# Performance work log

Measured on AMD Instinct MI355X. Metric: run time of the kernel, lower is better.

The kernel has to match this reference:

```python
import jax, jax.numpy as jnp
import numpy as np
import math

D_MODEL = 1024
EXPAND = 2
D_INNER = EXPAND * D_MODEL  # 2048
D_STATE = 16
D_CONV = 4
DT_RANK = math.ceil(D_MODEL / 16)  # 64
BATCH = 1
SEQLEN = 2048


def _silu(x):
    return x * jax.nn.sigmoid(x)


def _selective_scan(u, delta, A, B, C, D, z, delta_bias):
    """u, delta, z: (b,d,l); A: (d,n); B, C: (b,n,l); D, delta_bias: (d)."""
    delta = jax.nn.softplus(delta + delta_bias[None, :, None])        # (b,d,l)
    dA = jnp.exp(jnp.einsum('bdl,dn->lbdn', delta, A))                # (l,b,d,n)
    dBu = jnp.einsum('bdl,bnl->lbdn', delta * u, B)                   # (l,b,d,n)
    Ct = jnp.transpose(C, (2, 0, 1))                                  # (l,b,n)

    def step(h, inp):
        dA_t, dBu_t, C_t = inp
        h = dA_t * h + dBu_t                                          # (b,d,n)
        y = jnp.einsum('bdn,bn->bd', h, C_t)
        return h, y

    h0 = jnp.zeros((u.shape[0], u.shape[1], A.shape[1]), dtype=u.dtype)
    _, ys = jax.lax.scan(step, h0, (dA, dBu, Ct))                     # ys: (l,b,d)
    y = jnp.transpose(ys, (1, 2, 0))                                  # (b,d,l)
    y = y + D[:, None] * u
    return y * _silu(z)


def _causal_conv1d(x, conv_w, conv_b):
    """x: (b,d,l); conv_w: (d,w); conv_b: (d). Depthwise causal conv."""
    x_pad = jnp.pad(x, ((0, 0), (0, 0), (D_CONV - 1, 0)))
    kernel = conv_w[:, None, :]  # (d, 1, w)
    y = jax.lax.conv_general_dilated(
        x_pad, kernel, window_strides=(1,), padding='VALID',
        dimension_numbers=('NCH', 'OIH', 'NCH'),
        feature_group_count=D_INNER)
    return y + conv_b[None, :, None]


def setup_inputs() -> dict:
    key = jax.random.key(0)
    ks = jax.random.split(key, 12)
    hidden_states = jax.random.normal(ks[0], (BATCH, SEQLEN, D_MODEL), dtype=jnp.float32)
    in_proj_w = jax.random.normal(ks[1], (2 * D_INNER, D_MODEL), dtype=jnp.float32) * (D_MODEL ** -0.5)
    conv_w = jax.random.normal(ks[2], (D_INNER, D_CONV), dtype=jnp.float32) * (D_CONV ** -0.5)
    conv_b = jnp.zeros((D_INNER,), dtype=jnp.float32)
    dt_std = DT_RANK ** -0.5

    def dt_bias(k):
        dt = jnp.exp(jax.random.uniform(k, (D_INNER,)) * (math.log(0.1) - math.log(0.001)) + math.log(0.001))
        dt = jnp.clip(dt, 1e-4, None)
        return dt + jnp.log(-jnp.expm1(-dt))  # inverse softplus

    A_log = jnp.log(jnp.broadcast_to(jnp.arange(1, D_STATE + 1, dtype=jnp.float32), (D_INNER, D_STATE)))
    x1_proj_w = jax.random.normal(ks[3], (DT_RANK + 2 * D_STATE, D_INNER), dtype=jnp.float32) * (D_INNER ** -0.5)
    dt1_proj_w = jax.random.uniform(ks[4], (D_INNER, DT_RANK), minval=-dt_std, maxval=dt_std)
    dt1_proj_b = dt_bias(ks[5])
    x2_proj_w = jax.random.normal(ks[6], (DT_RANK + 2 * D_STATE, D_INNER), dtype=jnp.float32) * (D_INNER ** -0.5)
    dt2_proj_w = jax.random.uniform(ks[7], (D_INNER, DT_RANK), minval=-dt_std, maxval=dt_std)
    dt2_proj_b = dt_bias(ks[8])
    out_proj_w = jax.random.normal(ks[9], (D_MODEL, D_INNER), dtype=jnp.float32) * (D_INNER ** -0.5)
    return {
        'hidden_states': hidden_states,
        'in_proj_w': in_proj_w, 'conv_w': conv_w, 'conv_b': conv_b,
        'x1_proj_w': x1_proj_w, 'dt1_proj_w': dt1_proj_w, 'dt1_proj_b': dt1_proj_b,
        'A1_log': A_log, 'D1': jnp.ones((D_INNER,), dtype=jnp.float32),
        'x2_proj_w': x2_proj_w, 'dt2_proj_w': dt2_proj_w, 'dt2_proj_b': dt2_proj_b,
        'A2_log': A_log, 'D2': jnp.ones((D_INNER,), dtype=jnp.float32),
        'out_proj_w': out_proj_w,
    }


def reference(hidden_states, in_proj_w, conv_w, conv_b,
              x1_proj_w, dt1_proj_w, dt1_proj_b, A1_log, D1,
              x2_proj_w, dt2_proj_w, dt2_proj_b, A2_log, D2,
              out_proj_w):
    # in_proj: (b,l,d) @ W^T -> (b, 2*d_inner, l)
    xz = jnp.einsum('bld,ed->bel', hidden_states, in_proj_w)
    x, z = jnp.split(xz, 2, axis=1)                                   # (b,d_inner,l) each
    A1 = -jnp.exp(A1_log.astype(jnp.float32))
    A2 = -jnp.exp(A2_log.astype(jnp.float32))
    x = _silu(_causal_conv1d(x, conv_w, conv_b))                      # (b,d_inner,l)

    def branch_params(xp_w, dtp_w):
        dbl = jnp.einsum('bdl,kd->bkl', x, xp_w)                      # (b, r+2n, l)
        dt, Bm, Cm = jnp.split(dbl, [DT_RANK, DT_RANK + D_STATE], axis=1)
        dt = jnp.einsum('brl,dr->bdl', dt, dtp_w)
        return dt, Bm, Cm

    dt1, B1, C1 = branch_params(x1_proj_w, dt1_proj_w)
    dt2, B2, C2 = branch_params(x2_proj_w, dt2_proj_w)
    y1 = _selective_scan(x, dt1, A1, B1, C1, D1.astype(jnp.float32), z, dt1_proj_b.astype(jnp.float32))
    y2 = _selective_scan(x, dt2, A2, B2, C2, D2.astype(jnp.float32), z, dt2_proj_b.astype(jnp.float32))
    y = y1 - y2                                                       # (b,d_inner,l)
    out = jnp.einsum('bdl,od->blo', y, out_proj_w)                    # (b,l,d_model)
    return out
```

## Files before the change

kernel.cpp:

```cpp
#include <hip/hip_runtime.h>
#include <math.h>

#define SEQ 2048
#define DMODEL 1024
#define DIN 2048
#define NST 16
#define DTR 64
#define CH 64
#define NCH (SEQ / CH)

typedef __attribute__((ext_vector_type(8))) short bf16x8;
typedef __attribute__((ext_vector_type(4))) float f32x4;

__device__ __forceinline__ ushort f2bf(float f) {
  union { float f; unsigned u; } c; c.f = f;
  return (ushort)((c.u + 0x7fffu + ((c.u >> 16) & 1u)) >> 16);
}
__device__ __forceinline__ float bf2f(ushort h) {
  union { unsigned u; float f; } c; c.u = ((unsigned)h) << 16;
  return c.f;
}
__device__ __forceinline__ float splus(float v) {
  return v > 20.f ? v : log1pf(__expf(v));
}
__device__ __forceinline__ void powers16(float e, float* p) {
  float e2 = e * e, e4 = e2 * e2, e8 = e4 * e4;
  p[0] = e;       p[1] = e2;       p[2] = e2 * e;   p[3] = e4;
  p[4] = e4 * e;  p[5] = e4 * e2;  p[6] = e4 * p[2]; p[7] = e8;
  p[8] = e8 * e;  p[9] = e8 * e2;  p[10] = e8 * p[2]; p[11] = e8 * e4;
  p[12] = e8 * p[4]; p[13] = e8 * p[5]; p[14] = e8 * p[6]; p[15] = e8 * e8;
}

#define GLL(g, l) __builtin_amdgcn_global_load_lds( \
    (const __attribute__((address_space(1))) void*)(g), \
    (__attribute__((address_space(3))) void*)(l), 16, 0, 0)

template<int BM, int BN, int SPLITK>
__global__ __launch_bounds__(256) void gemm3p(const ushort* __restrict__ Ahi,
                                              const ushort* __restrict__ Alo,
                                              const ushort* __restrict__ Bhi,
                                              const ushort* __restrict__ Blo,
                                              float* __restrict__ C,
                                              int M, int N, int K) {
  constexpr int BK = 32;
  constexpr int WM = BM / 2, WN = BN / 2, TM = WM / 16, TN = WN / 16;
  constexpr int SA = BM / 16, SB = BN / 16;
  __shared__ __align__(16) ushort sAh[BM * BK], sAl[BM * BK];
  __shared__ __align__(16) ushort sBh[BN * BK], sBl[BN * BK];
  const int tid = threadIdx.x, wid = tid >> 6, lane = tid & 63;
  const int m0 = blockIdx.y * BM, n0 = blockIdx.x * BN;
  const int Kc = K / SPLITK, kbeg = blockIdx.z * Kc;
  const int wm0 = (wid >> 1) * WM, wn0 = (wid & 1) * WN;
  const int fr = lane & 15;
  const int lrow = lane >> 2;
  const int lkc = (lane & 3) ^ ((lane >> 3) & 3);
  const int fpo = fr * 32 + (((lane >> 4) ^ ((lane >> 1) & 3)) * 8);

  f32x4 acc[TM][TN];
#pragma unroll
  for (int mi = 0; mi < TM; ++mi)
#pragma unroll
    for (int ni = 0; ni < TN; ++ni)
#pragma unroll
      for (int r = 0; r < 4; ++r) acc[mi][ni][r] = 0.f;

  for (int k0 = 0; k0 < Kc; k0 += BK) {
    __syncthreads();
    const int kg = kbeg + k0 + lkc * 8;
#pragma unroll
    for (int i = 0; i < SA / 4; ++i) {
      const int seg = wid * (SA / 4) + i;
      const size_t ga = (size_t)(m0 + seg * 16 + lrow) * K + kg;
      GLL(&Ahi[ga], &sAh[seg * 512]);
      GLL(&Alo[ga], &sAl[seg * 512]);
    }
#pragma unroll
    for (int i = 0; i < SB / 4; ++i) {
      const int seg = wid * (SB / 4) + i;
      const size_t ga = (size_t)(n0 + seg * 16 + lrow) * K + kg;
      GLL(&Bhi[ga], &sBh[seg * 512]);
      GLL(&Blo[ga], &sBl[seg * 512]);
    }
    __syncthreads();

    bf16x8 ah[TM], al[TM], bh[TN], bl[TN];
#pragma unroll
    for (int mi = 0; mi < TM; ++mi) {
      const int r = (wm0 / 16 + mi) * 512 + fpo;
      ah[mi] = *(const bf16x8*)&sAh[r];
      al[mi] = *(const bf16x8*)&sAl[r];
    }
#pragma unroll
    for (int ni = 0; ni < TN; ++ni) {
      const int r = (wn0 / 16 + ni) * 512 + fpo;
      bh[ni] = *(const bf16x8*)&sBh[r];
      bl[ni] = *(const bf16x8*)&sBl[r];
    }
#pragma unroll
    for (int mi = 0; mi < TM; ++mi)
#pragma unroll
      for (int ni = 0; ni < TN; ++ni) {
        acc[mi][ni] = __builtin_amdgcn_mfma_f32_16x16x32_bf16(ah[mi], bh[ni], acc[mi][ni], 0, 0, 0);
        acc[mi][ni] = __builtin_amdgcn_mfma_f32_16x16x32_bf16(ah[mi], bl[ni], acc[mi][ni], 0, 0, 0);
        acc[mi][ni] = __builtin_amdgcn_mfma_f32_16x16x32_bf16(al[mi], bh[ni], acc[mi][ni], 0, 0, 0);
      }
  }

  float* __restrict__ Co = C + (size_t)blockIdx.z * M * N;
#pragma unroll
  for (int mi = 0; mi < TM; ++mi)
#pragma unroll
    for (int ni = 0; ni < TN; ++ni)
#pragma unroll
      for (int r = 0; r < 4; ++r)
        Co[(size_t)(m0 + wm0 + mi * 16 + (lane >> 4) * 4 + r) * N + n0 + wn0 + ni * 16 + fr] =
            acc[mi][ni][r];
}

__device__ __forceinline__ void split_store4(float4 v, ushort* hi, ushort* lo, size_t i) {
  ushort h0 = f2bf(v.x), h1 = f2bf(v.y), h2 = f2bf(v.z), h3 = f2bf(v.w);
  *(ushort4*)&hi[i] = make_ushort4(h0, h1, h2, h3);
  *(ushort4*)&lo[i] = make_ushort4(f2bf(v.x - bf2f(h0)), f2bf(v.y - bf2f(h1)),
                                   f2bf(v.z - bf2f(h2)), f2bf(v.w - bf2f(h3)));
}

__global__ __launch_bounds__(256) void cvt_fused(const float* __restrict__ inw,
                                                 const float* __restrict__ hid,
                                                 const float* __restrict__ x1w,
                                                 const float* __restrict__ x2w,
                                                 ushort* __restrict__ w_hi, ushort* __restrict__ w_lo,
                                                 ushort* __restrict__ h_hi, ushort* __restrict__ h_lo,
                                                 ushort* __restrict__ wx_hi, ushort* __restrict__ wx_lo) {
  const int q = blockIdx.x * 256 + threadIdx.x;
  const float* src; ushort* dhi; ushort* dlo; int base;
  if (q < 1048576)            { src = inw; dhi = w_hi;  dlo = w_lo;  base = q; }
  else if (q < 1572864)       { src = hid; dhi = h_hi;  dlo = h_lo;  base = q - 1048576; }
  else if (q < 1622016)       { src = x1w; dhi = wx_hi; dlo = wx_lo; base = q - 1572864; }
  else                        { src = x2w; dhi = wx_hi + 196608; dlo = wx_lo + 196608; base = q - 1622016; }
  const size_t i = (size_t)base * 4;
  split_store4(*(const float4*)&src[i], dhi, dlo, i);
}

__global__ __launch_bounds__(256) void cvt_split(const float* __restrict__ x,
                                                 ushort* __restrict__ hi,
                                                 ushort* __restrict__ lo, int n) {
  const int i = (blockIdx.x * 256 + threadIdx.x) * 4;
  if (i >= n) return;
  split_store4(*(const float4*)&x[i], hi, lo, i);
}

__global__ __launch_bounds__(256) void reduce_out(const float* __restrict__ p,
                                                  float* __restrict__ o, int n) {
  const int i = (blockIdx.x * 256 + threadIdx.x) * 4;
  if (i >= n) return;
  float4 a = *(const float4*)&p[i];
  float4 b = *(const float4*)&p[(size_t)n + i];
  float4 c = *(const float4*)&p[(size_t)2 * n + i];
  float4 d = *(const float4*)&p[(size_t)3 * n + i];
  *(float4*)&o[i] = make_float4(a.x + b.x + c.x + d.x, a.y + b.y + c.y + d.y,
                                a.z + b.z + c.z + d.z, a.w + b.w + c.w + d.w);
}

__global__ __launch_bounds__(256) void conv_tr_kernel(const float* __restrict__ xz,
                                                      const float* __restrict__ cw,
                                                      const float* __restrict__ cb,
                                                      ushort* __restrict__ xcT_hi,
                                                      ushort* __restrict__ xcT_lo) {
  const int l0 = blockIdx.x * 64, d0 = blockIdx.y * 64;
  const int tid = threadIdx.x;
  __shared__ float xin[64][68];
  __shared__ float To[64][65];
  __shared__ float cwS[64][4];
  __shared__ float cbS[64];

  for (int i = tid; i < 1024; i += 256) {
    const int d = i >> 4, q = i & 15;
    float4 v = *(const float4*)&xz[(size_t)(d0 + d) * SEQ + l0 + q * 4];
    xin[d][3 + q * 4 + 0] = v.x; xin[d][3 + q * 4 + 1] = v.y;
    xin[d][3 + q * 4 + 2] = v.z; xin[d][3 + q * 4 + 3] = v.w;
  }
  if (tid < 192) {
    const int j = tid >> 6, d = tid & 63;
    const int l = l0 - 3 + j;
    xin[d][j] = (l >= 0) ? xz[(size_t)(d0 + d) * SEQ + l] : 0.f;
  }
  if (tid < 64) {
    cbS[tid] = cb[d0 + tid];
    float4 w = *(const float4*)&cw[(d0 + tid) * 4];
    cwS[tid][0] = w.x; cwS[tid][1] = w.y; cwS[tid][2] = w.z; cwS[tid][3] = w.w;
  }
  __syncthreads();

  for (int i = tid; i < 4096; i += 256) {
    const int d = i >> 6, l = i & 63;
    float a = cbS[d] + cwS[d][0] * xin[d][l] + cwS[d][1] * xin[d][l + 1] +
              cwS[d][2] * xin[d][l + 2] + cwS[d][3] * xin[d][l + 3];
    To[d][l] = a / (1.f + __expf(-a));
  }
  __syncthreads();

  for (int i = tid; i < 4096; i += 256) {
    const int l = i >> 6, dd = i & 63;
    float v = To[dd][l];
    ushort h = f2bf(v);
    xcT_hi[(size_t)(l0 + l) * DIN + d0 + dd] = h;
    xcT_lo[(size_t)(l0 + l) * DIN + d0 + dd] = f2bf(v - bf2f(h));
  }
}

__global__ __launch_bounds__(256) void ydiff_tr_kernel(const float* __restrict__ y1,
                                                       const float* __restrict__ y2,
                                                       const float* __restrict__ xz,
                                                       ushort* __restrict__ hi,
                                                       ushort* __restrict__ lo) {
  const int l0 = blockIdx.x * 64, d0 = blockIdx.y * 64;
  const int tid = threadIdx.x;
  __shared__ float Tz[64][65];
  for (int i = tid; i < 1024; i += 256) {
    const int d = i >> 4, q = i & 15;
    float4 v = *(const float4*)&xz[(size_t)(DIN + d0 + d) * SEQ + l0 + q * 4];
    Tz[d][q * 4 + 0] = v.x / (1.f + __expf(-v.x));
    Tz[d][q * 4 + 1] = v.y / (1.f + __expf(-v.y));
    Tz[d][q * 4 + 2] = v.z / (1.f + __expf(-v.z));
    Tz[d][q * 4 + 3] = v.w / (1.f + __expf(-v.w));
  }
  __syncthreads();
  for (int i = tid; i < 1024; i += 256) {
    const int l = i >> 4, dc = (i & 15) * 4;
    const size_t g = (size_t)(l0 + l) * DIN + d0 + dc;
    float4 a = *(const float4*)&y1[g];
    float4 b = *(const float4*)&y2[g];
    float4 v = make_float4((a.x - b.x) * Tz[dc + 0][l], (a.y - b.y) * Tz[dc + 1][l],
                           (a.z - b.z) * Tz[dc + 2][l], (a.w - b.w) * Tz[dc + 3][l]);
    split_store4(v, hi, lo, g);
  }
}

__global__ __launch_bounds__(256) void reduce_dblS_kernel(const float* __restrict__ p,
                                                          float* __restrict__ o,
                                                          float* __restrict__ BT1,
                                                          float* __restrict__ CT1,
                                                          float* __restrict__ BT2,
                                                          float* __restrict__ CT2) {
  const int NE = 192 * SEQ;
  const int idx = blockIdx.x * 256 + threadIdx.x;
  float s = 0.f;
#pragma unroll
  for (int cc = 0; cc < 8; ++cc) s += p[(size_t)cc * NE + idx];
  o[idx] = s;
  const int k = idx >> 11, l = idx & (SEQ - 1);
  if (k >= 64 && k < 80)        BT1[l * NST + (k - 64)] = s;
  else if (k >= 80 && k < 96)   CT1[l * NST + (k - 80)] = s;
  else if (k >= 160 && k < 176) BT2[l * NST + (k - 160)] = s;
  else if (k >= 176)            CT2[l * NST + (k - 176)] = s;
}

__global__ __launch_bounds__(256) void dt_gemm_kernel(const float* __restrict__ dbl1,
                                                      const float* __restrict__ dbl2,
                                                      const float* __restrict__ w1,
                                                      const float* __restrict__ w2,
                                                      const float* __restrict__ b1,
                                                      const float* __restrict__ b2,
                                                      float* __restrict__ o1,
                                                      float* __restrict__ o2) {
  const int br = blockIdx.z;
  const float* __restrict__ dbl = br ? dbl2 : dbl1;
  const float* __restrict__ W = br ? w2 : w1;
  const float* __restrict__ dtb = br ? b2 : b1;
  float* __restrict__ outp = br ? o2 : o1;
  const int l0 = blockIdx.x * 64, d0 = blockIdx.y * 64;
  __shared__ __align__(16) float Wt[64][68];
  __shared__ __align__(16) float Bs[64][68];
  const int tid = threadIdx.x;
  for (int i = tid; i < 4096; i += 256) {
    int a = i >> 6, b = i & 63;
    Wt[b][a] = W[(size_t)(d0 + a) * DTR + b];
    Bs[a][b] = dbl[(size_t)a * SEQ + l0 + b];
  }
  __syncthreads();
  const int tl_ = tid >> 4, td_ = tid & 15;
  float acc[4][4];
#pragma unroll
  for (int i = 0; i < 4; ++i)
#pragma unroll
    for (int j = 0; j < 4; ++j) acc[i][j] = 0.f;
  for (int r = 0; r < 64; ++r) {
    float4 av = *(const float4*)&Bs[r][tl_ * 4];
    float4 bv = *(const float4*)&Wt[r][td_ * 4];
    float am[4] = {av.x, av.y, av.z, av.w};
    float bn[4] = {bv.x, bv.y, bv.z, bv.w};
#pragma unroll
    for (int i = 0; i < 4; ++i)
#pragma unroll
      for (int j = 0; j < 4; ++j) acc[i][j] = fmaf(am[i], bn[j], acc[i][j]);
  }
  const float4 bias4 = *(const float4*)&dtb[d0 + td_ * 4];
#pragma unroll
  for (int i = 0; i < 4; ++i) {
    float4 w = make_float4(splus(acc[i][0] + bias4.x), splus(acc[i][1] + bias4.y),
                           splus(acc[i][2] + bias4.z), splus(acc[i][3] + bias4.w));
    *(float4*)&outp[(size_t)(l0 + tl_ * 4 + i) * DIN + d0 + td_ * 4] = w;
  }
}

__global__ __launch_bounds__(256) void scan_phase_a(const ushort* __restrict__ uhi,
                                                    const ushort* __restrict__ ulo,
                                                    const float* __restrict__ sp1T,
                                                    const float* __restrict__ sp2T,
                                                    const float* __restrict__ BT1,
                                                    const float* __restrict__ BT2,
                                                    const float* __restrict__ Al1,
                                                    const float* __restrict__ Al2,
                                                    float* __restrict__ hend,
                                                    float* __restrict__ Pend) {
  const int br = blockIdx.z;
  const float* __restrict__ spp = br ? sp2T : sp1T;
  const float* __restrict__ BT = br ? BT2 : BT1;
  const float* __restrict__ Al = br ? Al2 : Al1;
  const int c = blockIdx.y;
  const int t0 = c * CH;
  const int d = blockIdx.x * 256 + threadIdx.x;
  const size_t gbase = (size_t)t0 * DIN + d;

  __shared__ __align__(16) float Bs[CH][NST];
  ((float4*)Bs)[threadIdx.x] = ((const float4*)&BT[t0 * NST])[threadIdx.x];
  __syncthreads();

  bool fast = true;
#pragma unroll
  for (int n = 0; n < NST; ++n) {
    float kx = __expf(Al[(size_t)d * NST + n]);
    fast = fast && (fabsf(kx - (float)(n + 1)) < 1e-3f);
  }
  float h[NST];
#pragma unroll
  for (int n = 0; n < NST; ++n) h[n] = 0.f;
  float S = 0.f;

  if (fast) {
    for (int tt = 0; tt < CH / 4; ++tt) {
      float sparr[4], uarr[4];
#pragma unroll
      for (int j = 0; j < 4; ++j) {
        const size_t idx = gbase + (size_t)(tt * 4 + j) * DIN;
        sparr[j] = spp[idx];
        uarr[j] = bf2f(uhi[idx]) + bf2f(ulo[idx]);
      }
#pragma unroll
      for (int j = 0; j < 4; ++j) {
        const int t = tt * 4 + j;
        const float sp = sparr[j];
        S += sp;
        const float spu = sp * uarr[j];
        const float e = __expf(-sp);
        float p[NST];
        powers16(e, p);
#pragma unroll
        for (int ng = 0; ng < 4; ++ng) {
          float4 bq = *(const float4*)&Bs[t][ng * 4];
          float bf[4] = {bq.x, bq.y, bq.z, bq.w};
#pragma unroll
          for (int k = 0; k < 4; ++k) {
            int n = ng * 4 + k;
            h[n] = fmaf(p[n], h[n], spu * bf[k]);
          }
        }
      }
    }
  } else {
    float AnL2[NST];
#pragma unroll
    for (int n = 0; n < NST; ++n)
      AnL2[n] = -__expf(Al[(size_t)d * NST + n]) * 1.4426950408889634f;
    for (int tt = 0; tt < CH / 4; ++tt) {
      float sparr[4], uarr[4];
#pragma unroll
      for (int j = 0; j < 4; ++j) {
        const size_t idx = gbase + (size_t)(tt * 4 + j) * DIN;
        sparr[j] = spp[idx];
        uarr[j] = bf2f(uhi[idx]) + bf2f(ulo[idx]);
      }
#pragma unroll
      for (int j = 0; j < 4; ++j) {
        const int t = tt * 4 + j;
        const float sp = sparr[j];
        S += sp;
        const float spu = sp * uarr[j];
#pragma unroll
        for (int ng = 0; ng < 4; ++ng) {
          float4 bq = *(const float4*)&Bs[t][ng * 4];
          float bf[4] = {bq.x, bq.y, bq.z, bq.w};
#pragma unroll
          for (int k = 0; k < 4; ++k) {
            int n = ng * 4 + k;
            float dA = exp2f(AnL2[n] * sp);
            h[n] = fmaf(dA, h[n], spu * bf[k]);
          }
        }
      }
    }
  }

  float P[NST];
  if (fast) {
    powers16(__expf(-S), P);
  } else {
#pragma unroll
    for (int n = 0; n < NST; ++n)
      P[n] = exp2f(-__expf(Al[(size_t)d * NST + n]) * 1.4426950408889634f * S);
  }
  size_t base = ((size_t)(br * NCH + c) * DIN + d) * NST;
#pragma unroll
  for (int n = 0; n < NST; n += 4) {
    *(float4*)&hend[base + n] = make_float4(h[n], h[n + 1], h[n + 2], h[n + 3]);
    *(float4*)&Pend[base + n] = make_float4(P[n], P[n + 1], P[n + 2], P[n + 3]);
  }
}

__global__ __launch_bounds__(256) void scan_carry(const float* __restrict__ hend,
                                                  float* __restrict__ PendHin) {
  const int flat = blockIdx.x * 256 + threadIdx.x;
  const int br = flat >> 15;
  const int dn = flat & 32767;
  float h = 0.f;
  for (int c = 0; c < NCH; ++c) {
    size_t idx = ((size_t)(br * NCH + c) << 15) + dn;
    float Pv = PendHin[idx];
    float he = hend[idx];
    PendHin[idx] = h;
    h = fmaf(Pv, h, he);
  }
}

__global__ __launch_bounds__(256) void scan_phase_c(const ushort* __restrict__ uhi,
                                                    const ushort* __restrict__ ulo,
                                                    const float* __restrict__ sp1T,
                                                    const float* __restrict__ sp2T,
                                                    const float* __restrict__ BT1,
                                                    const float* __restrict__ CT1,
                                                    const float* __restrict__ BT2,
                                                    const float* __restrict__ CT2,
                                                    const float* __restrict__ Al1,
                                                    const float* __restrict__ Al2,
                                                    const float* __restrict__ D1,
                                                    const float* __restrict__ D2,
                                                    const float* __restrict__ hin,
                                                    float* __restrict__ y1t,
                                                    float* __restrict__ y2t) {
  const int br = blockIdx.z;
  const float* __restrict__ spp = br ? sp2T : sp1T;
  const float* __restrict__ BT = br ? BT2 : BT1;
  const float* __restrict__ CT = br ? CT2 : CT1;
  const float* __restrict__ Al = br ? Al2 : Al1;
  const float* __restrict__ Dp = br ? D2 : D1;
  float* __restrict__ yt = br ? y2t : y1t;
  const int c = blockIdx.y;
  const int t0 = c * CH;
  const int d = blockIdx.x * 256 + threadIdx.x;
  const size_t gbase = (size_t)t0 * DIN + d;

  __shared__ __align__(16) float Bs[CH][NST];
  __shared__ __align__(16) float Cs[CH][NST];
  ((float4*)Bs)[threadIdx.x] = ((const float4*)&BT[t0 * NST])[threadIdx.x];
  ((float4*)Cs)[threadIdx.x] = ((const float4*)&CT[t0 * NST])[threadIdx.x];
  __syncthreads();

  bool fast = true;
#pragma unroll
  for (int n = 0; n < NST; ++n) {
    float kx = __expf(Al[(size_t)d * NST + n]);
    fast = fast && (fabsf(kx - (float)(n + 1)) < 1e-3f);
  }
  const float Dd = Dp[d];
  float h[NST];
  const size_t hbase = ((size_t)(br * NCH + c) * DIN + d) * NST;
#pragma unroll
  for (int n = 0; n < NST; n += 4) {
    float4 hv = *(const float4*)&hin[hbase + n];
    h[n] = hv.x; h[n + 1] = hv.y; h[n + 2] = hv.z; h[n + 3] = hv.w;
  }

  if (fast) {
    for (int tt = 0; tt < CH / 4; ++tt) {
      float sparr[4], uarr[4];
#pragma unroll
      for (int j = 0; j < 4; ++j) {
        const size_t idx = gbase + (size_t)(tt * 4 + j) * DIN;
        sparr[j] = spp[idx];
        uarr[j] = bf2f(uhi[idx]) + bf2f(ulo[idx]);
      }
#pragma unroll
      for (int j = 0; j < 4; ++j) {
        const int t = tt * 4 + j;
        const float sp = sparr[j];
        const float spu = sp * uarr[j];
        const float e = __expf(-sp);
        float p[NST];
        powers16(e, p);
        float y = 0.f;
#pragma unroll
        for (int ng = 0; ng < 4; ++ng) {
          float4 bq = *(const float4*)&Bs[t][ng * 4];
          float4 cq = *(const float4*)&Cs[t][ng * 4];
          float bf[4] = {bq.x, bq.y, bq.z, bq.w};
          float cf[4] = {cq.x, cq.y, cq.z, cq.w};
#pragma unroll
          for (int k = 0; k < 4; ++k) {
            int n = ng * 4 + k;
            h[n] = fmaf(p[n], h[n], spu * bf[k]);
            y = fmaf(h[n], cf[k], y);
          }
        }
        yt[gbase + (size_t)t * DIN] = y + Dd * uarr[j];
      }
    }
  } else {
    float AnL2[NST];
#pragma unroll
    for (int n = 0; n < NST; ++n)
      AnL2[n] = -__expf(Al[(size_t)d * NST + n]) * 1.4426950408889634f;
    for (int tt = 0; tt < CH / 4; ++tt) {
      float sparr[4], uarr[4];
#pragma unroll
      for (int j = 0; j < 4; ++j) {
        const size_t idx = gbase + (size_t)(tt * 4 + j) * DIN;
        sparr[j] = spp[idx];
        uarr[j] = bf2f(uhi[idx]) + bf2f(ulo[idx]);
      }
#pragma unroll
      for (int j = 0; j < 4; ++j) {
        const int t = tt * 4 + j;
        const float sp = sparr[j];
        const float spu = sp * uarr[j];
        float y = 0.f;
#pragma unroll
        for (int ng = 0; ng < 4; ++ng) {
          float4 bq = *(const float4*)&Bs[t][ng * 4];
          float4 cq = *(const float4*)&Cs[t][ng * 4];
          float bf[4] = {bq.x, bq.y, bq.z, bq.w};
          float cf[4] = {cq.x, cq.y, cq.z, cq.w};
#pragma unroll
          for (int k = 0; k < 4; ++k) {
            int n = ng * 4 + k;
            float dA = exp2f(AnL2[n] * sp);
            h[n] = fmaf(dA, h[n], spu * bf[k]);
            y = fmaf(h[n], cf[k], y);
          }
        }
        yt[gbase + (size_t)t * DIN] = y + Dd * uarr[j];
      }
    }
  }
}

extern "C" void kernel_launch(void* const* d_in, const int* in_sizes, int n_in,
                              void* d_out, int out_size, void* d_ws, size_t ws_size,
                              hipStream_t stream) {
  const float* hidden = (const float*)d_in[0];
  const float* in_proj_w = (const float*)d_in[1];
  const float* conv_w = (const float*)d_in[2];
  const float* conv_b = (const float*)d_in[3];
  const float* x1w = (const float*)d_in[4];
  const float* dtw1 = (const float*)d_in[5];
  const float* dtb1 = (const float*)d_in[6];
  const float* Al1 = (const float*)d_in[7];
  const float* D1 = (const float*)d_in[8];
  const float* x2w = (const float*)d_in[9];
  const float* dtw2 = (const float*)d_in[10];
  const float* dtb2 = (const float*)d_in[11];
  const float* Al2 = (const float*)d_in[12];
  const float* D2 = (const float*)d_in[13];
  const float* outw = (const float*)d_in[14];
  float* out = (float*)d_out;

  float* ws = (float*)d_ws;
  float* xz = ws;
  float* xcTbuf = xz + (size_t)4096 * SEQ;
  float* dblS = xcTbuf + (size_t)SEQ * DIN;
  float* sp1T = dblS + (size_t)192 * SEQ;
  float* sp2T = sp1T + (size_t)SEQ * DIN;
  float* y1t = sp2T + (size_t)SEQ * DIN;
  float* y2t = y1t + (size_t)SEQ * DIN;
  float* hend = y2t + (size_t)SEQ * DIN;
  float* Pend = hend + (size_t)2 * NCH * DIN * NST;
  float* BT1 = Pend + (size_t)2 * NCH * DIN * NST;
  float* CT1 = BT1 + (size_t)SEQ * NST;
  float* BT2 = CT1 + (size_t)SEQ * NST;
  float* CT2 = BT2 + (size_t)SEQ * NST;
  float* wxp = CT2 + (size_t)SEQ * NST;

  float* dbl1 = dblS;
  float* dbl2 = dblS + (size_t)96 * SEQ;

  ushort* xcT_hi = (ushort*)xcTbuf;
  ushort* xcT_lo = (ushort*)(xcTbuf + 2097152);
  ushort* w_hi = (ushort*)y1t;
  ushort* w_lo = (ushort*)(y1t + 2097152);
  ushort* h_hi = (ushort*)y2t;
  ushort* h_lo = (ushort*)(y2t + 1048576);
  ushort* wx_hi = (ushort*)wxp;
  ushort* wx_lo = (ushort*)(wxp + 196608);
  float* xp_part = sp1T;
  ushort* yd_hi = (ushort*)xcTbuf;
  ushort* yd_lo = (ushort*)(xcTbuf + 2097152);
  ushort* ow_hi = (ushort*)hend;
  ushort* ow_lo = (ushort*)(hend + 1048576);
  float* opart = xz;

  dim3 blk(256);

  cvt_fused<<<dim3(6528), blk, 0, stream>>>(in_proj_w, hidden, x1w, x2w,
                                            w_hi, w_lo, h_hi, h_lo, wx_hi, wx_lo);

  gemm3p<128, 128, 1><<<dim3(SEQ / 128, 4096 / 128, 1), blk, 0, stream>>>(
      w_hi, w_lo, h_hi, h_lo, xz, 4096, SEQ, DMODEL);

  conv_tr_kernel<<<dim3(SEQ / 64, DIN / 64), blk, 0, stream>>>(
      xz, conv_w, conv_b, xcT_hi, xcT_lo);

  gemm3p<64, 128, 8><<<dim3(SEQ / 128, 192 / 64, 8), blk, 0, stream>>>(
      wx_hi, wx_lo, xcT_hi, xcT_lo, xp_part, 192, SEQ, DIN);

  reduce_dblS_kernel<<<dim3(192 * SEQ / 256), blk, 0, stream>>>(
      xp_part, dblS, BT1, CT1, BT2, CT2);

  dt_gemm_kernel<<<dim3(SEQ / 64, DIN / 64, 2), blk, 0, stream>>>(
      dbl1, dbl2, dtw1, dtw2, dtb1, dtb2, sp1T, sp2T);

  scan_phase_a<<<dim3(DIN / 256, NCH, 2), blk, 0, stream>>>(
      xcT_hi, xcT_lo, sp1T, sp2T, BT1, BT2, Al1, Al2, hend, Pend);
  scan_carry<<<dim3(2 * DIN * NST / 256), blk, 0, stream>>>(hend, Pend);
  cvt_split<<<dim3(2048), blk, 0, stream>>>(outw, ow_hi, ow_lo, DMODEL * DIN);
  scan_phase_c<<<dim3(DIN / 256, NCH, 2), blk, 0, stream>>>(
      xcT_hi, xcT_lo, sp1T, sp2T, BT1, CT1, BT2, CT2, Al1, Al2, D1, D2, Pend, y1t, y2t);

  ydiff_tr_kernel<<<dim3(SEQ / 64, DIN / 64), blk, 0, stream>>>(
      y1t, y2t, xz, yd_hi, yd_lo);

  gemm3p<128, 128, 4><<<dim3(DMODEL / 128, SEQ / 128, 4), blk, 0, stream>>>(
      yd_hi, yd_lo, ow_hi, ow_lo, opart, SEQ, DMODEL, DIN);
  reduce_out<<<dim3(SEQ * DMODEL / 1024), blk, 0, stream>>>(opart, out, SEQ * DMODEL);
}
```

Baseline: 334.8 us.

## Fuse both scan branches with y-difference and gating into one phase-c kernel

The two selective-scan branches are computed in the same thread in one kernel, which also applies the y1-y2 difference, the silu(z) gate and the bf16 hi/lo split. This removes the y1/y2 intermediate round trip and the separate ydiff kernel. A new z transpose kernel precomputes silu(z) in (l,d) layout. The cost is half as many blocks and roughly doubled register pressure per thread.

```diff
diff --git a/kernel.cpp b/kernel.cpp
--- a/kernel.cpp
+++ b/kernel.cpp
@@ -208,11 +208,8 @@
   }
 }
 
-__global__ __launch_bounds__(256) void ydiff_tr_kernel(const float* __restrict__ y1,
-                                                       const float* __restrict__ y2,
-                                                       const float* __restrict__ xz,
-                                                       ushort* __restrict__ hi,
-                                                       ushort* __restrict__ lo) {
+__global__ __launch_bounds__(256) void z_tr_kernel(const float* __restrict__ xz,
+                                                   float* __restrict__ zT) {
   const int l0 = blockIdx.x * 64, d0 = blockIdx.y * 64;
   const int tid = threadIdx.x;
   __shared__ float Tz[64][65];
@@ -227,12 +224,8 @@
   __syncthreads();
   for (int i = tid; i < 1024; i += 256) {
     const int l = i >> 4, dc = (i & 15) * 4;
-    const size_t g = (size_t)(l0 + l) * DIN + d0 + dc;
-    float4 a = *(const float4*)&y1[g];
-    float4 b = *(const float4*)&y2[g];
-    float4 v = make_float4((a.x - b.x) * Tz[dc + 0][l], (a.y - b.y) * Tz[dc + 1][l],
-                           (a.z - b.z) * Tz[dc + 2][l], (a.w - b.w) * Tz[dc + 3][l]);
-    split_store4(v, hi, lo, g);
+    *(float4*)&zT[(size_t)(l0 + l) * DIN + d0 + dc] =
+        make_float4(Tz[dc + 0][l], Tz[dc + 1][l], Tz[dc + 2][l], Tz[dc + 3][l]);
   }
 }
 
@@ -432,122 +425,143 @@
   }
 }
 
-__global__ __launch_bounds__(256) void scan_phase_c(const ushort* __restrict__ uhi,
-                                                    const ushort* __restrict__ ulo,
-                                                    const float* __restrict__ sp1T,
-                                                    const float* __restrict__ sp2T,
-                                                    const float* __restrict__ BT1,
-                                                    const float* __restrict__ CT1,
-                                                    const float* __restrict__ BT2,
-                                                    const float* __restrict__ CT2,
-                                                    const float* __restrict__ Al1,
-                                                    const float* __restrict__ Al2,
-                                                    const float* __restrict__ D1,
-                                                    const float* __restrict__ D2,
-                                                    const float* __restrict__ hin,
-                                                    float* __restrict__ y1t,
-                                                    float* __restrict__ y2t) {
-  const int br = blockIdx.z;
-  const float* __restrict__ spp = br ? sp2T : sp1T;
-  const float* __restrict__ BT = br ? BT2 : BT1;
-  const float* __restrict__ CT = br ? CT2 : CT1;
-  const float* __restrict__ Al = br ? Al2 : Al1;
-  const float* __restrict__ Dp = br ? D2 : D1;
-  float* __restrict__ yt = br ? y2t : y1t;
+__global__ __launch_bounds__(256) void scan_phase_c_fused(
+    const ushort* __restrict__ uhi, const ushort* __restrict__ ulo,
+    const float* __restrict__ sp1T, const float* __restrict__ sp2T,
+    const float* __restrict__ BT1, const float* __restrict__ CT1,
+    const float* __restrict__ BT2, const float* __restrict__ CT2,
+    const float* __restrict__ Al1, const float* __restrict__ Al2,
+    const float* __restrict__ D1, const float* __restrict__ D2,
+    const float* __restrict__ hin, const float* __restrict__ zT,
+    ushort* __restrict__ yd_hi, ushort* __restrict__ yd_lo) {
   const int c = blockIdx.y;
   const int t0 = c * CH;
   const int d = blockIdx.x * 256 + threadIdx.x;
   const size_t gbase = (size_t)t0 * DIN + d;
 
-  __shared__ __align__(16) float Bs[CH][NST];
-  __shared__ __align__(16) float Cs[CH][NST];
-  ((float4*)Bs)[threadIdx.x] = ((const float4*)&BT[t0 * NST])[threadIdx.x];
-  ((float4*)Cs)[threadIdx.x] = ((const float4*)&CT[t0 * NST])[threadIdx.x];
+  __shared__ __align__(16) float Bs1[CH][NST], Cs1[CH][NST];
+  __shared__ __align__(16) float Bs2[CH][NST], Cs2[CH][NST];
+  ((float4*)Bs1)[threadIdx.x] = ((const float4*)&BT1[t0 * NST])[threadIdx.x];
+  ((float4*)Cs1)[threadIdx.x] = ((const float4*)&CT1[t0 * NST])[threadIdx.x];
+  ((float4*)Bs2)[threadIdx.x] = ((const float4*)&BT2[t0 * NST])[threadIdx.x];
+  ((float4*)Cs2)[threadIdx.x] = ((const float4*)&CT2[t0 * NST])[threadIdx.x];
   __syncthreads();
 
   bool fast = true;
 #pragma unroll
   for (int n = 0; n < NST; ++n) {
-    float kx = __expf(Al[(size_t)d * NST + n]);
-    fast = fast && (fabsf(kx - (float)(n + 1)) < 1e-3f);
-  }
-  const float Dd = Dp[d];
-  float h[NST];
-  const size_t hbase = ((size_t)(br * NCH + c) * DIN + d) * NST;
+    float k1 = __expf(Al1[(size_t)d * NST + n]);
+    float k2 = __expf(Al2[(size_t)d * NST + n]);
+    fast = fast && (fabsf(k1 - (float)(n + 1)) < 1e-3f) &&
+           (fabsf(k2 - (float)(n + 1)) < 1e-3f);
+  }
+  const float Dd1 = D1[d], Dd2 = D2[d];
+  float h1[NST], h2[NST];
+  const size_t hb1 = ((size_t)c * DIN + d) * NST;
+  const size_t hb2 = ((size_t)(NCH + c) * DIN + d) * NST;
 #pragma unroll
   for (int n = 0; n < NST; n += 4) {
-    float4 hv = *(const float4*)&hin[hbase + n];
-    h[n] = hv.x; h[n + 1] = hv.y; h[n + 2] = hv.z; h[n + 3] = hv.w;
+    float4 v1 = *(const float4*)&hin[hb1 + n];
+    float4 v2 = *(const float4*)&hin[hb2 + n];
+    h1[n] = v1.x; h1[n + 1] = v1.y; h1[n + 2] = v1.z; h1[n + 3] = v1.w;
+    h2[n] = v2.x; h2[n + 1] = v2.y; h2[n + 2] = v2.z; h2[n + 3] = v2.w;
   }
 
   if (fast) {
     for (int tt = 0; tt < CH / 4; ++tt) {
-      float sparr[4], uarr[4];
+      float sp1a[4], sp2a[4], uarr[4], zarr[4];
 #pragma unroll
       for (int j = 0; j < 4; ++j) {
         const size_t idx = gbase + (size_t)(tt * 4 + j) * DIN;
-        sparr[j] = spp[idx];
+        sp1a[j] = sp1T[idx];
+        sp2a[j] = sp2T[idx];
         uarr[j] = bf2f(uhi[idx]) + bf2f(ulo[idx]);
+        zarr[j] = zT[idx];
       }
 #pragma unroll
       for (int j = 0; j < 4; ++j) {
         const int t = tt * 4 + j;
-        const float sp = sparr[j];
-        const float spu = sp * uarr[j];
-        const float e = __expf(-sp);
-        float p[NST];
-        powers16(e, p);
-        float y = 0.f;
+        const float uu = uarr[j];
+        const float spu1 = sp1a[j] * uu, spu2 = sp2a[j] * uu;
+        float p1[NST], p2[NST];
+        powers16(__expf(-sp1a[j]), p1);
+        powers16(__expf(-sp2a[j]), p2);
+        float y1 = 0.f, y2 = 0.f;
 #pragma unroll
         for (int ng = 0; ng < 4; ++ng) {
-          float4 bq = *(const float4*)&Bs[t][ng * 4];
-          float4 cq = *(const float4*)&Cs[t][ng * 4];
-          float bf[4] = {bq.x, bq.y, bq.z, bq.w};
-          float cf[4] = {cq.x, cq.y, cq.z, cq.w};
+          float4 b1 = *(const float4*)&Bs1[t][ng * 4];
+          float4 c1 = *(const float4*)&Cs1[t][ng * 4];
+          float4 b2 = *(const float4*)&Bs2[t][ng * 4];
+          float4 c2 = *(const float4*)&Cs2[t][ng * 4];
+          float b1f[4] = {b1.x, b1.y, b1.z, b1.w};
+          float c1f[4] = {c1.x, c1.y, c1.z, c1.w};
+          float b2f[4] = {b2.x, b2.y, b2.z, b2.w};
+          float c2f[4] = {c2.x, c2.y, c2.z, c2.w};
 #pragma unroll
           for (int k = 0; k < 4; ++k) {
             int n = ng * 4 + k;
-            h[n] = fmaf(p[n], h[n], spu * bf[k]);
-            y = fmaf(h[n], cf[k], y);
+            h1[n] = fmaf(p1[n], h1[n], spu1 * b1f[k]);
+            y1 = fmaf(h1[n], c1f[k], y1);
+            h2[n] = fmaf(p2[n], h2[n], spu2 * b2f[k]);
+            y2 = fmaf(h2[n], c2f[k], y2);
           }
         }
-        yt[gbase + (size_t)t * DIN] = y + Dd * uarr[j];
+        const float v = ((y1 + Dd1 * uu) - (y2 + Dd2 * uu)) * zarr[j];
+        const size_t oi = gbase + (size_t)t * DIN;
+        ushort hh = f2bf(v);
+        yd_hi[oi] = hh;
+        yd_lo[oi] = f2bf(v - bf2f(hh));
       }
     }
   } else {
-    float AnL2[NST];
-#pragma unroll
-    for (int n = 0; n < NST; ++n)
-      AnL2[n] = -__expf(Al[(size_t)d * NST + n]) * 1.4426950408889634f;
+    float A1L2[NST], A2L2[NST];
+#pragma unroll
+    for (int n = 0; n < NST; ++n) {
+      A1L2[n] = -__expf(Al1[(size_t)d * NST + n]) * 1.4426950408889634f;
+      A2L2[n] = -__expf(Al2[(size_t)d * NST + n]) * 1.4426950408889634f;
+    }
     for (int tt = 0; tt < CH / 4; ++tt) {
-      float sparr[4], uarr[4];
+      float sp1a[4], sp2a[4], uarr[4], zarr[4];
 #pragma unroll
       for (int j = 0; j < 4; ++j) {
         const size_t idx = gbase + (size_t)(tt * 4 + j) * DIN;
-        sparr[j] = spp[idx];
+        sp1a[j] = sp1T[idx];
+        sp2a[j] = sp2T[idx];
         uarr[j] = bf2f(uhi[idx]) + bf2f(ulo[idx]);
+        zarr[j] = zT[idx];
       }
 #pragma unroll
       for (int j = 0; j < 4; ++j) {
         const int t = tt * 4 + j;
-        const float sp = sparr[j];
-        const float spu = sp * uarr[j];
-        float y = 0.f;
+        const float uu = uarr[j];
+        const float spu1 = sp1a[j] * uu, spu2 = sp2a[j] * uu;
+        float y1 = 0.f, y2 = 0.f;
 #pragma unroll
         for (int ng = 0; ng < 4; ++ng) {
-          float4 bq = *(const float4*)&Bs[t][ng * 4];
-          float4 cq = *(const float4*)&Cs[t][ng * 4];
-          float bf[4] = {bq.x, bq.y, bq.z, bq.w};
-          float cf[4] = {cq.x, cq.y, cq.z, cq.w};
+          float4 b1 = *(const float4*)&Bs1[t][ng * 4];
+          float4 c1 = *(const float4*)&Cs1[t][ng * 4];
+          float4 b2 = *(const float4*)&Bs2[t][ng * 4];
+          float4 c2 = *(const float4*)&Cs2[t][ng * 4];
+          float b1f[4] = {b1.x, b1.y, b1.z, b1.w};
+          float c1f[4] = {c1.x, c1.y, c1.z, c1.w};
+          float b2f[4] = {b2.x, b2.y, b2.z, b2.w};
+          float c2f[4] = {c2.x, c2.y, c2.z, c2.w};
 #pragma unroll
           for (int k = 0; k < 4; ++k) {
             int n = ng * 4 + k;
-            float dA = exp2f(AnL2[n] * sp);
-            h[n] = fmaf(dA, h[n], spu * bf[k]);
-            y = fmaf(h[n], cf[k], y);
+            float dA1 = exp2f(A1L2[n] * sp1a[j]);
+            float dA2 = exp2f(A2L2[n] * sp2a[j]);
+            h1[n] = fmaf(dA1, h1[n], spu1 * b1f[k]);
+            y1 = fmaf(h1[n], c1f[k], y1);
+            h2[n] = fmaf(dA2, h2[n], spu2 * b2f[k]);
+            y2 = fmaf(h2[n], c2f[k], y2);
           }
         }
-        yt[gbase + (size_t)t * DIN] = y + Dd * uarr[j];
+        const float v = ((y1 + Dd1 * uu) - (y2 + Dd2 * uu)) * zarr[j];
+        const size_t oi = gbase + (size_t)t * DIN;
+        ushort hh = f2bf(v);
+        yd_hi[oi] = hh;
+        yd_lo[oi] = f2bf(v - bf2f(hh));
       }
     }
   }
@@ -601,8 +615,9 @@
   ushort* wx_hi = (ushort*)wxp;
   ushort* wx_lo = (ushort*)(wxp + 196608);
   float* xp_part = sp1T;
-  ushort* yd_hi = (ushort*)xcTbuf;
-  ushort* yd_lo = (ushort*)(xcTbuf + 2097152);
+  float* zT = y1t;
+  ushort* yd_hi = (ushort*)y2t;
+  ushort* yd_lo = (ushort*)(y2t + 2097152);
   ushort* ow_hi = (ushort*)hend;
   ushort* ow_lo = (ushort*)(hend + 1048576);
   float* opart = xz;
@@ -617,6 +632,7 @@
 
   conv_tr_kernel<<<dim3(SEQ / 64, DIN / 64), blk, 0, stream>>>(
       xz, conv_w, conv_b, xcT_hi, xcT_lo);
+  z_tr_kernel<<<dim3(SEQ / 64, DIN / 64), blk, 0, stream>>>(xz, zT);
 
   gemm3p<64, 128, 8><<<dim3(SEQ / 128, 192 / 64, 8), blk, 0, stream>>>(
       wx_hi, wx_lo, xcT_hi, xcT_lo, xp_part, 192, SEQ, DIN);
@@ -631,11 +647,9 @@
       xcT_hi, xcT_lo, sp1T, sp2T, BT1, BT2, Al1, Al2, hend, Pend);
   scan_carry<<<dim3(2 * DIN * NST / 256), blk, 0, stream>>>(hend, Pend);
   cvt_split<<<dim3(2048), blk, 0, stream>>>(outw, ow_hi, ow_lo, DMODEL * DIN);
-  scan_phase_c<<<dim3(DIN / 256, NCH, 2), blk, 0, stream>>>(
-      xcT_hi, xcT_lo, sp1T, sp2T, BT1, CT1, BT2, CT2, Al1, Al2, D1, D2, Pend, y1t, y2t);
-
-  ydiff_tr_kernel<<<dim3(SEQ / 64, DIN / 64), blk, 0, stream>>>(
-      y1t, y2t, xz, yd_hi, yd_lo);
+  scan_phase_c_fused<<<dim3(DIN / 256, NCH), blk, 0, stream>>>(
+      xcT_hi, xcT_lo, sp1T, sp2T, BT1, CT1, BT2, CT2, Al1, Al2, D1, D2,
+      Pend, zT, yd_hi, yd_lo);
 
   gemm3p<128, 128, 4><<<dim3(DMODEL / 128, SEQ / 128, 4), blk, 0, stream>>>(
       yd_hi, yd_lo, ow_hi, ow_lo, opart, SEQ, DMODEL, DIN);
```

After: 344.4 us. 1.03x slower.
